# Optimization experiments

Measured on AMD Instinct MI355X. Metric: run time of the kernel, lower is better.

## Reference

```python
import jax, jax.numpy as jnp
import numpy as np

B, S, K, V = 512, 1024, 128, 512
SCALE = float(np.sqrt(K))


def setup_inputs() -> dict:
    key0 = jax.random.key(0)
    ks = jax.random.split(key0, 16)
    inp = {
        "keys": jax.random.normal(ks[0], (B, S, K), jnp.float32),
        "values": jax.random.normal(ks[1], (B, S, V), jnp.float32),
        "key": jax.random.normal(ks[2], (B, K), jnp.float32),
        "value": jax.random.normal(ks[3], (B, V), jnp.float32),
        "hidden": jax.random.normal(ks[4], (B, V), jnp.float32),
        "write_ptr": jax.random.randint(ks[5], (B,), 0, S, jnp.int64).astype(jnp.int64),
        "filled": jax.random.randint(ks[6], (B,), 0, S, jnp.int64).astype(jnp.int64),
        # parameters (Linear: y = x @ W.T + b)
        "Wq": jax.random.normal(ks[7], (K, V), jnp.float32) / np.sqrt(V),
        "bq": jnp.zeros((K,), jnp.float32),
        "Wg1": jax.random.normal(ks[8], (V, 2 * V), jnp.float32) / np.sqrt(2 * V),
        "bg1": jnp.zeros((V,), jnp.float32),
        "Wg2": jax.random.normal(ks[9], (V, V), jnp.float32) / np.sqrt(V),
        "bg2": jnp.zeros((V,), jnp.float32),
        "Wo": jax.random.normal(ks[10], (V, V), jnp.float32) / np.sqrt(V),
        "bo": jnp.zeros((V,), jnp.float32),
    }
    return inp


def reference(keys, values, key, value, hidden, write_ptr, filled,
              Wq, bq, Wg1, bg1, Wg2, bg2, Wo, bo):
    b_idx = jnp.arange(B)
    # --- write (ring-buffer scatter; torch does it under no_grad) ---
    keys_w = keys.at[b_idx, write_ptr].set(jax.lax.stop_gradient(key))
    values_w = values.at[b_idx, write_ptr].set(jax.lax.stop_gradient(value))
    filled_w = jnp.minimum(filled + 1, S)
    # --- read ---
    query = hidden @ Wq.T + bq                                  # (B, K)
    scores = jnp.einsum('bsk,bk->bs', keys_w, query) / SCALE     # (B, S)
    valid = jnp.arange(S)[None, :] < filled_w[:, None]           # (B, S)
    scores = jnp.where(valid, scores, -jnp.inf)
    attn = jax.nn.softmax(scores, axis=-1)
    attn = jnp.nan_to_num(attn, nan=0.0)
    retrieved = jnp.einsum('bs,bsv->bv', attn, values_w)         # (B, V)
    h_cat = jnp.concatenate([hidden, retrieved], axis=-1)        # (B, 2V)
    g = jax.nn.silu(h_cat @ Wg1.T + bg1)
    gate = jax.nn.sigmoid(g @ Wg2.T + bg2)
    out = (hidden + gate * retrieved) @ Wo.T + bo                # (B, V)
    return out
```

## Files before the change

kernel.cpp:

```cpp
#include <hip/hip_runtime.h>
#include <math.h>

#define BB 512
#define SS 1024
#define KK 128
#define VV 512
#define NC 4
#define CH 256

static constexpr float INV_SCALE = 0.088388347648318447f;

__global__ __launch_bounds__(128) void q_kernel(
    const float* __restrict__ hidden, const float* __restrict__ Wq,
    const float* __restrict__ bq, float* __restrict__ qout)
{
    __shared__ __align__(16) float hid[VV];
    const int b = blockIdx.x, t = threadIdx.x;
    ((float4*)hid)[t] = ((const float4*)(hidden + (size_t)b * VV))[t];
    __syncthreads();
    const float4* w4 = (const float4*)(Wq + (size_t)t * VV);
    const float4* h4 = (const float4*)hid;
    float acc = 0.f;
    #pragma unroll 8
    for (int v = 0; v < VV / 4; ++v) {
        float4 a = w4[v], h = h4[v];
        acc += a.x * h.x + a.y * h.y + a.z * h.z + a.w * h.w;
    }
    qout[(size_t)b * KK + t] = acc + bq[t];
}

__global__ __launch_bounds__(256) void transpose3_kernel(
    const float* __restrict__ Wg1, const float* __restrict__ Wg2,
    const float* __restrict__ Wo,
    float* __restrict__ wt1, float* __restrict__ wt2, float* __restrict__ wto)
{
    __shared__ float tile[32][33];
    const int idx = blockIdx.x;
    const float* in; float* out; int C, R, tid;
    if (idx < 512)      { in = Wg1; out = wt1; R = 512; C = 1024; tid = idx; }
    else if (idx < 768) { in = Wg2; out = wt2; R = 512; C = 512;  tid = idx - 512; }
    else                { in = Wo;  out = wto; R = 512; C = 512;  tid = idx - 768; }
    const int tiles_x = C >> 5;
    const int bx = (tid % tiles_x) << 5;
    const int by = (tid / tiles_x) << 5;
    const int tx = threadIdx.x & 31, ty0 = threadIdx.x >> 5;
    #pragma unroll
    for (int i = 0; i < 32; i += 8)
        tile[ty0 + i][tx] = in[(size_t)(by + ty0 + i) * C + bx + tx];
    __syncthreads();
    #pragma unroll
    for (int i = 0; i < 32; i += 8)
        out[(size_t)(bx + ty0 + i) * R + by + tx] = tile[tx][ty0 + i];
}

__global__ __launch_bounds__(256) void attn_chunk_kernel(
    const float* __restrict__ keys, const float* __restrict__ values,
    const float* __restrict__ keyv, const float* __restrict__ valv,
    const float* __restrict__ q,
    const int* __restrict__ write_ptr, const int* __restrict__ filled,
    float* __restrict__ ml, float* __restrict__ accp)
{
    __shared__ __align__(16) float qs[KK];
    __shared__ __align__(16) float p[CH];
    __shared__ __align__(16) float red[4];
    __shared__ __align__(16) float4 pvp[VV / 4];

    const int bc = blockIdx.x;
    const int b = bc >> 2;
    const int c = bc & 3;
    const int t = threadIdx.x;
    const int wave = t >> 6, lane = t & 63;

    int f = filled[b] + 1; if (f > SS) f = SS;
    const int sbeg = c * CH;
    int n = f - sbeg; if (n > CH) n = CH;

    float* mlrow = ml + ((size_t)b * NC + c) * 2;
    float* arow  = accp + ((size_t)b * NC + c) * VV;

    if (n <= 0) {
        if (t == 0) { mlrow[0] = -INFINITY; mlrow[1] = 0.f; }
        if (t < VV / 4) ((float4*)arow)[t] = make_float4(0.f, 0.f, 0.f, 0.f);
        return;
    }

    if (t < KK / 4) ((float4*)qs)[t] = ((const float4*)(q + (size_t)b * KK))[t];
    __syncthreads();

    const int sub = lane & 31, rsel = lane >> 5;
    const int srow = wave * 2 + rsel;
    const float4 q4 = ((const float4*)qs)[sub];
    const float* kb = keys + ((size_t)b * SS + sbeg) * KK;
    const float* kw = keyv + (size_t)b * KK;
    const int wpl = write_ptr[b] - sbeg;

    const int nmain = n & ~31;
    for (int s0 = 0; s0 < nmain; s0 += 32) {
        float4 kv[4];
        #pragma unroll
        for (int u = 0; u < 4; ++u) {
            const int s = s0 + u * 8 + srow;
            const float* kr = (s == wpl) ? kw : (kb + (size_t)s * KK);
            kv[u] = ((const float4*)kr)[sub];
        }
        #pragma unroll
        for (int u = 0; u < 4; ++u) {
            float prt = kv[u].x * q4.x + kv[u].y * q4.y
                      + kv[u].z * q4.z + kv[u].w * q4.w;
            prt += __shfl_xor(prt, 16);
            prt += __shfl_xor(prt, 8);
            prt += __shfl_xor(prt, 4);
            prt += __shfl_xor(prt, 2);
            prt += __shfl_xor(prt, 1);
            if (sub == 0) p[s0 + u * 8 + srow] = prt * INV_SCALE;
        }
    }
    for (int s = nmain + srow; s < n; s += 8) {
        const float* kr = (s == wpl) ? kw : (kb + (size_t)s * KK);
        const float4 kv = ((const float4*)kr)[sub];
        float prt = kv.x * q4.x + kv.y * q4.y + kv.z * q4.z + kv.w * q4.w;
        prt += __shfl_xor(prt, 16);
        prt += __shfl_xor(prt, 8);
        prt += __shfl_xor(prt, 4);
        prt += __shfl_xor(prt, 2);
        prt += __shfl_xor(prt, 1);
        if (sub == 0) p[s] = prt * INV_SCALE;
    }
    __syncthreads();

    float lmax = -INFINITY;
    for (int i = t; i < n; i += 256) lmax = fmaxf(lmax, p[i]);
    lmax = fmaxf(lmax, __shfl_xor(lmax, 32));
    lmax = fmaxf(lmax, __shfl_xor(lmax, 16));
    lmax = fmaxf(lmax, __shfl_xor(lmax, 8));
    lmax = fmaxf(lmax, __shfl_xor(lmax, 4));
    lmax = fmaxf(lmax, __shfl_xor(lmax, 2));
    lmax = fmaxf(lmax, __shfl_xor(lmax, 1));
    if (lane == 0) red[wave] = lmax;
    __syncthreads();
    const float m = fmaxf(fmaxf(red[0], red[1]), fmaxf(red[2], red[3]));
    float lsum = 0.f;
    for (int i = t; i < n; i += 256) {
        const float e = __expf(p[i] - m);
        p[i] = e;
        lsum += e;
    }
    lsum += __shfl_xor(lsum, 32);
    lsum += __shfl_xor(lsum, 16);
    lsum += __shfl_xor(lsum, 8);
    lsum += __shfl_xor(lsum, 4);
    lsum += __shfl_xor(lsum, 2);
    lsum += __shfl_xor(lsum, 1);
    __syncthreads();
    if (lane == 0) red[wave] = lsum;
    __syncthreads();
    const float l = red[0] + red[1] + red[2] + red[3];

    const int col4 = t & 127, stream = t >> 7;
    const float4* vb = (const float4*)(values + ((size_t)b * SS + sbeg) * VV);
    const float4* vw = (const float4*)(valv + (size_t)b * VV);
    float4 acc = make_float4(0.f, 0.f, 0.f, 0.f);
    const int nm2 = n & ~15;
    for (int s0 = 0; s0 < nm2; s0 += 16) {
        float4 v[8]; float ps[8];
        #pragma unroll
        for (int u = 0; u < 8; ++u) {
            const int s = s0 + u * 2 + stream;
            const float4* vr = (s == wpl) ? vw : (vb + (size_t)s * (VV / 4));
            v[u] = vr[col4];
            ps[u] = p[s];
        }
        #pragma unroll
        for (int u = 0; u < 8; ++u) {
            acc.x += ps[u] * v[u].x;
            acc.y += ps[u] * v[u].y;
            acc.z += ps[u] * v[u].z;
            acc.w += ps[u] * v[u].w;
        }
    }
    for (int s = nm2 + stream; s < n; s += 2) {
        const float4* vr = (s == wpl) ? vw : (vb + (size_t)s * (VV / 4));
        const float4 v = vr[col4];
        const float psv = p[s];
        acc.x += psv * v.x;
        acc.y += psv * v.y;
        acc.z += psv * v.z;
        acc.w += psv * v.w;
    }
    if (stream == 1) pvp[col4] = acc;
    __syncthreads();
    if (stream == 0) {
        const float4 o = pvp[col4];
        ((float4*)arow)[col4] = make_float4(acc.x + o.x, acc.y + o.y,
                                            acc.z + o.z, acc.w + o.w);
    }
    if (t == 0) { mlrow[0] = m; mlrow[1] = l; }
}

__global__ __launch_bounds__(128) void combine_kernel(
    const float* __restrict__ hidden, const float* __restrict__ ml,
    const float* __restrict__ accp, float* __restrict__ hcat)
{
    const int b = blockIdx.x, t = threadIdx.x;
    const float* mlb = ml + (size_t)b * NC * 2;
    const float m0 = mlb[0], l0 = mlb[1], m1 = mlb[2], l1 = mlb[3];
    const float m2 = mlb[4], l2 = mlb[5], m3 = mlb[6], l3 = mlb[7];
    const float ms = fmaxf(fmaxf(m0, m1), fmaxf(m2, m3));
    const float w0 = __expf(m0 - ms), w1 = __expf(m1 - ms);
    const float w2 = __expf(m2 - ms), w3 = __expf(m3 - ms);
    const float invd = 1.f / (w0 * l0 + w1 * l1 + w2 * l2 + w3 * l3);
    const float4 x0 = ((const float4*)(accp + ((size_t)b * NC + 0) * VV))[t];
    const float4 x1 = ((const float4*)(accp + ((size_t)b * NC + 1) * VV))[t];
    const float4 x2 = ((const float4*)(accp + ((size_t)b * NC + 2) * VV))[t];
    const float4 x3 = ((const float4*)(accp + ((size_t)b * NC + 3) * VV))[t];
    float4 r;
    r.x = (w0 * x0.x + w1 * x1.x + w2 * x2.x + w3 * x3.x) * invd;
    r.y = (w0 * x0.y + w1 * x1.y + w2 * x2.y + w3 * x3.y) * invd;
    r.z = (w0 * x0.z + w1 * x1.z + w2 * x2.z + w3 * x3.z) * invd;
    r.w = (w0 * x0.w + w1 * x1.w + w2 * x2.w + w3 * x3.w) * invd;
    float4* hc = (float4*)(hcat + (size_t)b * 2 * VV);
    hc[t] = ((const float4*)(hidden + (size_t)b * VV))[t];
    hc[VV / 4 + t] = r;
}

__global__ __launch_bounds__(256) void gemm_ks_kernel(
    const float* __restrict__ A, int K, const float* __restrict__ B,
    float* __restrict__ part)
{
    __shared__ __align__(16) float As[16][68];
    __shared__ __align__(16) float Bs[16][68];
    const int bx = blockIdx.x;
    const int mt = bx & 7, nt = (bx >> 3) & 7, ks = bx >> 6;
    const int kseg = K >> 2;
    const int kbeg = ks * kseg, kend = kbeg + kseg;
    const int t = threadIdx.x;
    const int tx = t & 15, ty = t >> 4;
    const int m0 = mt << 6, n0 = nt << 6;
    const int ra = t >> 2, ca = (t & 3) << 2;
    const int rb = t >> 4, jb = (t & 15) << 2;
    float4 a0 = {0,0,0,0}, a1 = {0,0,0,0}, a2 = {0,0,0,0}, a3 = {0,0,0,0};

    for (int k0 = kbeg; k0 < kend; k0 += 16) {
        const float4 av = *(const float4*)(A + (size_t)(m0 + ra) * K + k0 + ca);
        const float4 bv = *(const float4*)(B + (size_t)(k0 + rb) * VV + n0 + jb);
        As[ca + 0][ra] = av.x;
        As[ca + 1][ra] = av.y;
        As[ca + 2][ra] = av.z;
        As[ca + 3][ra] = av.w;
        *(float4*)&Bs[rb][jb] = bv;
        __syncthreads();
        #pragma unroll
        for (int k = 0; k < 16; ++k) {
            const float4 a = *(const float4*)&As[k][ty << 2];
            const float4 b = *(const float4*)&Bs[k][tx << 2];
            a0.x += a.x * b.x; a0.y += a.x * b.y; a0.z += a.x * b.z; a0.w += a.x * b.w;
            a1.x += a.y * b.x; a1.y += a.y * b.y; a1.z += a.y * b.z; a1.w += a.y * b.w;
            a2.x += a.z * b.x; a2.y += a.z * b.y; a2.z += a.z * b.z; a2.w += a.z * b.w;
            a3.x += a.w * b.x; a3.y += a.w * b.y; a3.z += a.w * b.z; a3.w += a.w * b.w;
        }
        __syncthreads();
    }
    float* pp = part + ((size_t)(ks * 512 + m0 + (ty << 2))) * 512 + n0 + (tx << 2);
    *(float4*)(pp + 0 * 512) = a0;
    *(float4*)(pp + 1 * 512) = a1;
    *(float4*)(pp + 2 * 512) = a2;
    *(float4*)(pp + 3 * 512) = a3;
}

__global__ __launch_bounds__(128) void reduce_silu_kernel(
    const float* __restrict__ part, const float* __restrict__ bg1,
    float* __restrict__ G)
{
    const int b = blockIdx.x, t = threadIdx.x;
    const size_t o = (size_t)b * (VV / 4) + t;
    const size_t st = (size_t)512 * (VV / 4);
    const float4* p4 = (const float4*)part;
    const float4 s0 = p4[o], s1 = p4[o + st], s2 = p4[o + 2 * st], s3 = p4[o + 3 * st];
    const float4 bb = ((const float4*)bg1)[t];
    float4 s;
    s.x = s0.x + s1.x + s2.x + s3.x + bb.x;
    s.y = s0.y + s1.y + s2.y + s3.y + bb.y;
    s.z = s0.z + s1.z + s2.z + s3.z + bb.z;
    s.w = s0.w + s1.w + s2.w + s3.w + bb.w;
    float4 g;
    g.x = s.x / (1.f + __expf(-s.x));
    g.y = s.y / (1.f + __expf(-s.y));
    g.z = s.z / (1.f + __expf(-s.z));
    g.w = s.w / (1.f + __expf(-s.w));
    ((float4*)G)[o] = g;
}

__global__ __launch_bounds__(128) void reduce_gate_kernel(
    const float* __restrict__ part, const float* __restrict__ bg2,
    const float* __restrict__ hcat, float* __restrict__ X)
{
    const int b = blockIdx.x, t = threadIdx.x;
    const size_t o = (size_t)b * (VV / 4) + t;
    const size_t st = (size_t)512 * (VV / 4);
    const float4* p4 = (const float4*)part;
    const float4 s0 = p4[o], s1 = p4[o + st], s2 = p4[o + 2 * st], s3 = p4[o + 3 * st];
    const float4 bb = ((const float4*)bg2)[t];
    float4 s;
    s.x = s0.x + s1.x + s2.x + s3.x + bb.x;
    s.y = s0.y + s1.y + s2.y + s3.y + bb.y;
    s.z = s0.z + s1.z + s2.z + s3.z + bb.z;
    s.w = s0.w + s1.w + s2.w + s3.w + bb.w;
    const float4* hc = (const float4*)(hcat + (size_t)b * 2 * VV);
    const float4 h = hc[t];
    const float4 r = hc[VV / 4 + t];
    float4 x;
    x.x = h.x + r.x / (1.f + __expf(-s.x));
    x.y = h.y + r.y / (1.f + __expf(-s.y));
    x.z = h.z + r.z / (1.f + __expf(-s.z));
    x.w = h.w + r.w / (1.f + __expf(-s.w));
    ((float4*)X)[o] = x;
}

__global__ __launch_bounds__(128) void reduce_bias_kernel(
    const float* __restrict__ part, const float* __restrict__ bo,
    float* __restrict__ out)
{
    const int b = blockIdx.x, t = threadIdx.x;
    const size_t o = (size_t)b * (VV / 4) + t;
    const size_t st = (size_t)512 * (VV / 4);
    const float4* p4 = (const float4*)part;
    const float4 s0 = p4[o], s1 = p4[o + st], s2 = p4[o + 2 * st], s3 = p4[o + 3 * st];
    const float4 bb = ((const float4*)bo)[t];
    float4 s;
    s.x = s0.x + s1.x + s2.x + s3.x + bb.x;
    s.y = s0.y + s1.y + s2.y + s3.y + bb.y;
    s.z = s0.z + s1.z + s2.z + s3.z + bb.z;
    s.w = s0.w + s1.w + s2.w + s3.w + bb.w;
    ((float4*)out)[o] = s;
}

extern "C" void kernel_launch(void* const* d_in, const int* in_sizes, int n_in,
                              void* d_out, int out_size, void* d_ws, size_t ws_size,
                              hipStream_t stream) {
    const float* keys    = (const float*)d_in[0];
    const float* values  = (const float*)d_in[1];
    const float* keyv    = (const float*)d_in[2];
    const float* valv    = (const float*)d_in[3];
    const float* hidden  = (const float*)d_in[4];
    const int*   wptr    = (const int*)d_in[5];
    const int*   filled  = (const int*)d_in[6];
    const float* Wq  = (const float*)d_in[7];
    const float* bq  = (const float*)d_in[8];
    const float* Wg1 = (const float*)d_in[9];
    const float* bg1 = (const float*)d_in[10];
    const float* Wg2 = (const float*)d_in[11];
    const float* bg2 = (const float*)d_in[12];
    const float* Wo  = (const float*)d_in[13];
    const float* bo  = (const float*)d_in[14];
    float* out = (float*)d_out;

    float* ws   = (float*)d_ws;
    float* q    = ws;
    float* ml   = q + (size_t)BB * KK;
    float* accp = ml + (size_t)BB * NC * 2;
    float* wt1  = accp + (size_t)BB * NC * VV;
    float* wt2  = wt1 + (size_t)2 * VV * VV;
    float* wto  = wt2 + (size_t)VV * VV;
    float* hcat = wto + (size_t)VV * VV;
    float* G    = hcat + (size_t)BB * 2 * VV;
    float* X    = G + (size_t)BB * VV;
    float* part = X + (size_t)BB * VV;

    q_kernel<<<BB, 128, 0, stream>>>(hidden, Wq, bq, q);
    transpose3_kernel<<<1024, 256, 0, stream>>>(Wg1, Wg2, Wo, wt1, wt2, wto);
    attn_chunk_kernel<<<BB * NC, 256, 0, stream>>>(keys, values, keyv, valv, q,
                                                   wptr, filled, ml, accp);
    combine_kernel<<<BB, 128, 0, stream>>>(hidden, ml, accp, hcat);

    gemm_ks_kernel<<<256, 256, 0, stream>>>(hcat, 2 * VV, wt1, part);
    reduce_silu_kernel<<<BB, 128, 0, stream>>>(part, bg1, G);

    gemm_ks_kernel<<<256, 256, 0, stream>>>(G, VV, wt2, part);
    reduce_gate_kernel<<<BB, 128, 0, stream>>>(part, bg2, hcat, X);

    gemm_ks_kernel<<<256, 256, 0, stream>>>(X, VV, wto, part);
    reduce_bias_kernel<<<BB, 128, 0, stream>>>(part, bo, out);
}
```

Measured before the change: 231.4 us.

## Fuse split-K reduction into GEMM via atomic counters, merge prep kernels, double chunks

Merges the Q projection and weight transposes into one prep kernel, with the Q dot product split across two halves per block. Attention chunks go from 4 to 8 per batch row, giving more blocks for the memory-bound scan. The GEMMs go from 4-way to 8-way split-K, and the last-arriving block per tile, detected with an atomic counter and threadfence, sums the partials and applies the bias, SiLU, gate or identity epilogue. This removes the three reduce kernel launches, at the cost of a larger partial buffer, an extra memset and serialized tail work in the last block of each tile.

```diff
diff --git a/kernel.cpp b/kernel.cpp
--- a/kernel.cpp
+++ b/kernel.cpp
@@ -5,52 +5,58 @@
 #define SS 1024
 #define KK 128
 #define VV 512
-#define NC 4
-#define CH 256
+#define NC 8
+#define CH 128
+#define KS 8
 
 static constexpr float INV_SCALE = 0.088388347648318447f;
 
-__global__ __launch_bounds__(128) void q_kernel(
+__global__ __launch_bounds__(256) void prep_kernel(
+    const float* __restrict__ Wg1, const float* __restrict__ Wg2,
+    const float* __restrict__ Wo,
+    float* __restrict__ wt1, float* __restrict__ wt2, float* __restrict__ wto,
     const float* __restrict__ hidden, const float* __restrict__ Wq,
     const float* __restrict__ bq, float* __restrict__ qout)
 {
+    __shared__ float tile[32][33];
     __shared__ __align__(16) float hid[VV];
-    const int b = blockIdx.x, t = threadIdx.x;
-    ((float4*)hid)[t] = ((const float4*)(hidden + (size_t)b * VV))[t];
-    __syncthreads();
-    const float4* w4 = (const float4*)(Wq + (size_t)t * VV);
-    const float4* h4 = (const float4*)hid;
-    float acc = 0.f;
-    #pragma unroll 8
-    for (int v = 0; v < VV / 4; ++v) {
-        float4 a = w4[v], h = h4[v];
-        acc += a.x * h.x + a.y * h.y + a.z * h.z + a.w * h.w;
-    }
-    qout[(size_t)b * KK + t] = acc + bq[t];
-}
-
-__global__ __launch_bounds__(256) void transpose3_kernel(
-    const float* __restrict__ Wg1, const float* __restrict__ Wg2,
-    const float* __restrict__ Wo,
-    float* __restrict__ wt1, float* __restrict__ wt2, float* __restrict__ wto)
-{
-    __shared__ float tile[32][33];
+    __shared__ float qp[2][KK];
     const int idx = blockIdx.x;
-    const float* in; float* out; int C, R, tid;
-    if (idx < 512)      { in = Wg1; out = wt1; R = 512; C = 1024; tid = idx; }
-    else if (idx < 768) { in = Wg2; out = wt2; R = 512; C = 512;  tid = idx - 512; }
-    else                { in = Wo;  out = wto; R = 512; C = 512;  tid = idx - 768; }
-    const int tiles_x = C >> 5;
-    const int bx = (tid % tiles_x) << 5;
-    const int by = (tid / tiles_x) << 5;
-    const int tx = threadIdx.x & 31, ty0 = threadIdx.x >> 5;
-    #pragma unroll
-    for (int i = 0; i < 32; i += 8)
-        tile[ty0 + i][tx] = in[(size_t)(by + ty0 + i) * C + bx + tx];
-    __syncthreads();
-    #pragma unroll
-    for (int i = 0; i < 32; i += 8)
-        out[(size_t)(bx + ty0 + i) * R + by + tx] = tile[tx][ty0 + i];
+    const int t = threadIdx.x;
+    if (idx < 1024) {
+        const float* in; float* out; int C, R, tid;
+        if (idx < 512)      { in = Wg1; out = wt1; R = 512; C = 1024; tid = idx; }
+        else if (idx < 768) { in = Wg2; out = wt2; R = 512; C = 512;  tid = idx - 512; }
+        else                { in = Wo;  out = wto; R = 512; C = 512;  tid = idx - 768; }
+        const int tiles_x = C >> 5;
+        const int bx = (tid % tiles_x) << 5;
+        const int by = (tid / tiles_x) << 5;
+        const int tx = t & 31, ty0 = t >> 5;
+        #pragma unroll
+        for (int i = 0; i < 32; i += 8)
+            tile[ty0 + i][tx] = in[(size_t)(by + ty0 + i) * C + bx + tx];
+        __syncthreads();
+        #pragma unroll
+        for (int i = 0; i < 32; i += 8)
+            out[(size_t)(bx + ty0 + i) * R + by + tx] = tile[tx][ty0 + i];
+    } else {
+        const int b = idx - 1024;
+        if (t < VV / 4)
+            ((float4*)hid)[t] = ((const float4*)(hidden + (size_t)b * VV))[t];
+        __syncthreads();
+        const int k = t & 127, half = t >> 7;
+        const float4* w4 = (const float4*)(Wq + (size_t)k * VV + half * 256);
+        const float4* h4 = (const float4*)(hid + half * 256);
+        float acc = 0.f;
+        #pragma unroll 8
+        for (int v = 0; v < 64; ++v) {
+            float4 a = w4[v], h = h4[v];
+            acc += a.x * h.x + a.y * h.y + a.z * h.z + a.w * h.w;
+        }
+        qp[half][k] = acc;
+        __syncthreads();
+        if (t < KK) qout[(size_t)b * KK + t] = qp[0][t] + qp[1][t] + bq[t];
+    }
 }
 
 __global__ __launch_bounds__(256) void attn_chunk_kernel(
@@ -66,8 +72,8 @@
     __shared__ __align__(16) float4 pvp[VV / 4];
 
     const int bc = blockIdx.x;
-    const int b = bc >> 2;
-    const int c = bc & 3;
+    const int b = bc >> 3;
+    const int c = bc & 7;
     const int t = threadIdx.x;
     const int wave = t >> 6, lane = t & 63;
 
@@ -203,35 +209,42 @@
 {
     const int b = blockIdx.x, t = threadIdx.x;
     const float* mlb = ml + (size_t)b * NC * 2;
-    const float m0 = mlb[0], l0 = mlb[1], m1 = mlb[2], l1 = mlb[3];
-    const float m2 = mlb[4], l2 = mlb[5], m3 = mlb[6], l3 = mlb[7];
-    const float ms = fmaxf(fmaxf(m0, m1), fmaxf(m2, m3));
-    const float w0 = __expf(m0 - ms), w1 = __expf(m1 - ms);
-    const float w2 = __expf(m2 - ms), w3 = __expf(m3 - ms);
-    const float invd = 1.f / (w0 * l0 + w1 * l1 + w2 * l2 + w3 * l3);
-    const float4 x0 = ((const float4*)(accp + ((size_t)b * NC + 0) * VV))[t];
-    const float4 x1 = ((const float4*)(accp + ((size_t)b * NC + 1) * VV))[t];
-    const float4 x2 = ((const float4*)(accp + ((size_t)b * NC + 2) * VV))[t];
-    const float4 x3 = ((const float4*)(accp + ((size_t)b * NC + 3) * VV))[t];
-    float4 r;
-    r.x = (w0 * x0.x + w1 * x1.x + w2 * x2.x + w3 * x3.x) * invd;
-    r.y = (w0 * x0.y + w1 * x1.y + w2 * x2.y + w3 * x3.y) * invd;
-    r.z = (w0 * x0.z + w1 * x1.z + w2 * x2.z + w3 * x3.z) * invd;
-    r.w = (w0 * x0.w + w1 * x1.w + w2 * x2.w + w3 * x3.w) * invd;
+    float mv[NC], lv[NC];
+    #pragma unroll
+    for (int c = 0; c < NC; ++c) { mv[c] = mlb[2 * c]; lv[c] = mlb[2 * c + 1]; }
+    float ms = mv[0];
+    #pragma unroll
+    for (int c = 1; c < NC; ++c) ms = fmaxf(ms, mv[c]);
+    float w[NC], denom = 0.f;
+    #pragma unroll
+    for (int c = 0; c < NC; ++c) { w[c] = __expf(mv[c] - ms); denom += w[c] * lv[c]; }
+    const float invd = 1.f / denom;
+    float4 r = make_float4(0.f, 0.f, 0.f, 0.f);
+    #pragma unroll
+    for (int c = 0; c < NC; ++c) {
+        const float4 x = ((const float4*)(accp + ((size_t)b * NC + c) * VV))[t];
+        r.x += w[c] * x.x; r.y += w[c] * x.y; r.z += w[c] * x.z; r.w += w[c] * x.w;
+    }
+    r.x *= invd; r.y *= invd; r.z *= invd; r.w *= invd;
     float4* hc = (float4*)(hcat + (size_t)b * 2 * VV);
     hc[t] = ((const float4*)(hidden + (size_t)b * VV))[t];
     hc[VV / 4 + t] = r;
 }
 
-__global__ __launch_bounds__(256) void gemm_ks_kernel(
+__global__ __launch_bounds__(256) void gemm_ep_kernel(
     const float* __restrict__ A, int K, const float* __restrict__ B,
-    float* __restrict__ part)
+    float* __restrict__ part, int* __restrict__ cnt,
+    const float* __restrict__ bias, const float* __restrict__ hcat,
+    float* __restrict__ dst, int epi)
 {
     __shared__ __align__(16) float As[16][68];
     __shared__ __align__(16) float Bs[16][68];
+    __shared__ int lastFlag;
     const int bx = blockIdx.x;
-    const int mt = bx & 7, nt = (bx >> 3) & 7, ks = bx >> 6;
-    const int kseg = K >> 2;
+    const int tile_id = bx & 63;
+    const int ks = bx >> 6;
+    const int mt = tile_id & 7, nt = tile_id >> 3;
+    const int kseg = K >> 3;
     const int kbeg = ks * kseg, kend = kbeg + kseg;
     const int t = threadIdx.x;
     const int tx = t & 15, ty = t >> 4;
@@ -260,78 +273,51 @@
         }
         __syncthreads();
     }
-    float* pp = part + ((size_t)(ks * 512 + m0 + (ty << 2))) * 512 + n0 + (tx << 2);
-    *(float4*)(pp + 0 * 512) = a0;
-    *(float4*)(pp + 1 * 512) = a1;
-    *(float4*)(pp + 2 * 512) = a2;
-    *(float4*)(pp + 3 * 512) = a3;
-}
-
-__global__ __launch_bounds__(128) void reduce_silu_kernel(
-    const float* __restrict__ part, const float* __restrict__ bg1,
-    float* __restrict__ G)
-{
-    const int b = blockIdx.x, t = threadIdx.x;
-    const size_t o = (size_t)b * (VV / 4) + t;
-    const size_t st = (size_t)512 * (VV / 4);
-    const float4* p4 = (const float4*)part;
-    const float4 s0 = p4[o], s1 = p4[o + st], s2 = p4[o + 2 * st], s3 = p4[o + 3 * st];
-    const float4 bb = ((const float4*)bg1)[t];
-    float4 s;
-    s.x = s0.x + s1.x + s2.x + s3.x + bb.x;
-    s.y = s0.y + s1.y + s2.y + s3.y + bb.y;
-    s.z = s0.z + s1.z + s2.z + s3.z + bb.z;
-    s.w = s0.w + s1.w + s2.w + s3.w + bb.w;
-    float4 g;
-    g.x = s.x / (1.f + __expf(-s.x));
-    g.y = s.y / (1.f + __expf(-s.y));
-    g.z = s.z / (1.f + __expf(-s.z));
-    g.w = s.w / (1.f + __expf(-s.w));
-    ((float4*)G)[o] = g;
-}
-
-__global__ __launch_bounds__(128) void reduce_gate_kernel(
-    const float* __restrict__ part, const float* __restrict__ bg2,
-    const float* __restrict__ hcat, float* __restrict__ X)
-{
-    const int b = blockIdx.x, t = threadIdx.x;
-    const size_t o = (size_t)b * (VV / 4) + t;
-    const size_t st = (size_t)512 * (VV / 4);
-    const float4* p4 = (const float4*)part;
-    const float4 s0 = p4[o], s1 = p4[o + st], s2 = p4[o + 2 * st], s3 = p4[o + 3 * st];
-    const float4 bb = ((const float4*)bg2)[t];
-    float4 s;
-    s.x = s0.x + s1.x + s2.x + s3.x + bb.x;
-    s.y = s0.y + s1.y + s2.y + s3.y + bb.y;
-    s.z = s0.z + s1.z + s2.z + s3.z + bb.z;
-    s.w = s0.w + s1.w + s2.w + s3.w + bb.w;
-    const float4* hc = (const float4*)(hcat + (size_t)b * 2 * VV);
-    const float4 h = hc[t];
-    const float4 r = hc[VV / 4 + t];
-    float4 x;
-    x.x = h.x + r.x / (1.f + __expf(-s.x));
-    x.y = h.y + r.y / (1.f + __expf(-s.y));
-    x.z = h.z + r.z / (1.f + __expf(-s.z));
-    x.w = h.w + r.w / (1.f + __expf(-s.w));
-    ((float4*)X)[o] = x;
-}
-
-__global__ __launch_bounds__(128) void reduce_bias_kernel(
-    const float* __restrict__ part, const float* __restrict__ bo,
-    float* __restrict__ out)
-{
-    const int b = blockIdx.x, t = threadIdx.x;
-    const size_t o = (size_t)b * (VV / 4) + t;
-    const size_t st = (size_t)512 * (VV / 4);
-    const float4* p4 = (const float4*)part;
-    const float4 s0 = p4[o], s1 = p4[o + st], s2 = p4[o + 2 * st], s3 = p4[o + 3 * st];
-    const float4 bb = ((const float4*)bo)[t];
-    float4 s;
-    s.x = s0.x + s1.x + s2.x + s3.x + bb.x;
-    s.y = s0.y + s1.y + s2.y + s3.y + bb.y;
-    s.z = s0.z + s1.z + s2.z + s3.z + bb.z;
-    s.w = s0.w + s1.w + s2.w + s3.w + bb.w;
-    ((float4*)out)[o] = s;
+    const size_t st = (size_t)VV * VV;
+    {
+        float* pp = part + (size_t)ks * st
+                  + (size_t)(m0 + (ty << 2)) * VV + n0 + (tx << 2);
+        *(float4*)(pp + 0 * VV) = a0;
+        *(float4*)(pp + 1 * VV) = a1;
+        *(float4*)(pp + 2 * VV) = a2;
+        *(float4*)(pp + 3 * VV) = a3;
+    }
+    __threadfence();
+    if (t == 0) lastFlag = (atomicAdd(&cnt[tile_id], 1) == KS - 1);
+    __syncthreads();
+    if (!lastFlag) return;
+    __threadfence();
+
+    const int col = n0 + (tx << 2);
+    const float4 bb = *(const float4*)(bias + col);
+    #pragma unroll
+    for (int r = 0; r < 4; ++r) {
+        const int row = m0 + (ty << 2) + r;
+        float4 s = bb;
+        #pragma unroll
+        for (int k2 = 0; k2 < KS; ++k2) {
+            const float4 pv = *(const float4*)(part + (size_t)k2 * st
+                                               + (size_t)row * VV + col);
+            s.x += pv.x; s.y += pv.y; s.z += pv.z; s.w += pv.w;
+        }
+        float4 o;
+        if (epi == 0) {
+            o.x = s.x / (1.f + __expf(-s.x));
+            o.y = s.y / (1.f + __expf(-s.y));
+            o.z = s.z / (1.f + __expf(-s.z));
+            o.w = s.w / (1.f + __expf(-s.w));
+        } else if (epi == 1) {
+            const float4 h  = *(const float4*)(hcat + (size_t)row * (2 * VV) + col);
+            const float4 rr = *(const float4*)(hcat + (size_t)row * (2 * VV) + VV + col);
+            o.x = h.x + rr.x / (1.f + __expf(-s.x));
+            o.y = h.y + rr.y / (1.f + __expf(-s.y));
+            o.z = h.z + rr.z / (1.f + __expf(-s.z));
+            o.w = h.w + rr.w / (1.f + __expf(-s.w));
+        } else {
+            o = s;
+        }
+        *(float4*)(dst + (size_t)row * VV + col) = o;
+    }
 }
 
 extern "C" void kernel_launch(void* const* d_in, const int* in_sizes, int n_in,
@@ -365,19 +351,19 @@
     float* G    = hcat + (size_t)BB * 2 * VV;
     float* X    = G + (size_t)BB * VV;
     float* part = X + (size_t)BB * VV;
-
-    q_kernel<<<BB, 128, 0, stream>>>(hidden, Wq, bq, q);
-    transpose3_kernel<<<1024, 256, 0, stream>>>(Wg1, Wg2, Wo, wt1, wt2, wto);
+    int*   cnt  = (int*)(part + (size_t)KS * VV * VV);
+
+    hipMemsetAsync(cnt, 0, 3 * 64 * sizeof(int), stream);
+    prep_kernel<<<1536, 256, 0, stream>>>(Wg1, Wg2, Wo, wt1, wt2, wto,
+                                          hidden, Wq, bq, q);
     attn_chunk_kernel<<<BB * NC, 256, 0, stream>>>(keys, values, keyv, valv, q,
                                                    wptr, filled, ml, accp);
     combine_kernel<<<BB, 128, 0, stream>>>(hidden, ml, accp, hcat);
 
-    gemm_ks_kernel<<<256, 256, 0, stream>>>(hcat, 2 * VV, wt1, part);
-    reduce_silu_kernel<<<BB, 128, 0, stream>>>(part, bg1, G);
-
-    gemm_ks_kernel<<<256, 256, 0, stream>>>(G, VV, wt2, part);
-    reduce_gate_kernel<<<BB, 128, 0, stream>>>(part, bg2, hcat, X);
-
-    gemm_ks_kernel<<<256, 256, 0, stream>>>(X, VV, wto, part);
-    reduce_bias_kernel<<<BB, 128, 0, stream>>>(part, bo, out);
-}
+    gemm_ep_kernel<<<64 * KS, 256, 0, stream>>>(hcat, 2 * VV, wt1, part,
+                                                cnt, bg1, nullptr, G, 0);
+    gemm_ep_kernel<<<64 * KS, 256, 0, stream>>>(G, VV, wt2, part,
+                                                cnt + 64, bg2, hcat, X, 1);
+    gemm_ep_kernel<<<64 * KS, 256, 0, stream>>>(X, VV, wto, part,
+                                                cnt + 128, bo, nullptr, out, 2);
+}
```

Measured after the change: 387.3 us. 67.4% more time.

## Split attention into 16 chunks and read GEMM weights untransposed

Applied to the files above, without the earlier changes.

Attention is now split into 16 chunks of 64 keys per batch row instead of 4 chunks of 256, which gives more blocks and better load balance across the variable fill lengths. The combine step is generalised to merge 16 partial softmax results. The weight transpose kernel is removed, and the GEMM loads each W row directly and transposes it into shared memory the same way it does for A. This drops one launch and the transpose traffic, at the cost of strided W loads, more partial buffers and a heavier combine.

```diff
diff --git a/kernel.cpp b/kernel.cpp
--- a/kernel.cpp
+++ b/kernel.cpp
@@ -5,8 +5,9 @@
 #define SS 1024
 #define KK 128
 #define VV 512
-#define NC 4
-#define CH 256
+#define NC 16
+#define CH 64
+#define KS 4
 
 static constexpr float INV_SCALE = 0.088388347648318447f;
 
@@ -29,30 +30,6 @@
     qout[(size_t)b * KK + t] = acc + bq[t];
 }
 
-__global__ __launch_bounds__(256) void transpose3_kernel(
-    const float* __restrict__ Wg1, const float* __restrict__ Wg2,
-    const float* __restrict__ Wo,
-    float* __restrict__ wt1, float* __restrict__ wt2, float* __restrict__ wto)
-{
-    __shared__ float tile[32][33];
-    const int idx = blockIdx.x;
-    const float* in; float* out; int C, R, tid;
-    if (idx < 512)      { in = Wg1; out = wt1; R = 512; C = 1024; tid = idx; }
-    else if (idx < 768) { in = Wg2; out = wt2; R = 512; C = 512;  tid = idx - 512; }
-    else                { in = Wo;  out = wto; R = 512; C = 512;  tid = idx - 768; }
-    const int tiles_x = C >> 5;
-    const int bx = (tid % tiles_x) << 5;
-    const int by = (tid / tiles_x) << 5;
-    const int tx = threadIdx.x & 31, ty0 = threadIdx.x >> 5;
-    #pragma unroll
-    for (int i = 0; i < 32; i += 8)
-        tile[ty0 + i][tx] = in[(size_t)(by + ty0 + i) * C + bx + tx];
-    __syncthreads();
-    #pragma unroll
-    for (int i = 0; i < 32; i += 8)
-        out[(size_t)(bx + ty0 + i) * R + by + tx] = tile[tx][ty0 + i];
-}
-
 __global__ __launch_bounds__(256) void attn_chunk_kernel(
     const float* __restrict__ keys, const float* __restrict__ values,
     const float* __restrict__ keyv, const float* __restrict__ valv,
@@ -66,8 +43,8 @@
     __shared__ __align__(16) float4 pvp[VV / 4];
 
     const int bc = blockIdx.x;
-    const int b = bc >> 2;
-    const int c = bc & 3;
+    const int b = bc >> 4;
+    const int c = bc & 15;
     const int t = threadIdx.x;
     const int wave = t >> 6, lane = t & 63;
 
@@ -203,28 +180,30 @@
 {
     const int b = blockIdx.x, t = threadIdx.x;
     const float* mlb = ml + (size_t)b * NC * 2;
-    const float m0 = mlb[0], l0 = mlb[1], m1 = mlb[2], l1 = mlb[3];
-    const float m2 = mlb[4], l2 = mlb[5], m3 = mlb[6], l3 = mlb[7];
-    const float ms = fmaxf(fmaxf(m0, m1), fmaxf(m2, m3));
-    const float w0 = __expf(m0 - ms), w1 = __expf(m1 - ms);
-    const float w2 = __expf(m2 - ms), w3 = __expf(m3 - ms);
-    const float invd = 1.f / (w0 * l0 + w1 * l1 + w2 * l2 + w3 * l3);
-    const float4 x0 = ((const float4*)(accp + ((size_t)b * NC + 0) * VV))[t];
-    const float4 x1 = ((const float4*)(accp + ((size_t)b * NC + 1) * VV))[t];
-    const float4 x2 = ((const float4*)(accp + ((size_t)b * NC + 2) * VV))[t];
-    const float4 x3 = ((const float4*)(accp + ((size_t)b * NC + 3) * VV))[t];
-    float4 r;
-    r.x = (w0 * x0.x + w1 * x1.x + w2 * x2.x + w3 * x3.x) * invd;
-    r.y = (w0 * x0.y + w1 * x1.y + w2 * x2.y + w3 * x3.y) * invd;
-    r.z = (w0 * x0.z + w1 * x1.z + w2 * x2.z + w3 * x3.z) * invd;
-    r.w = (w0 * x0.w + w1 * x1.w + w2 * x2.w + w3 * x3.w) * invd;
+    float mv[NC], lv[NC];
+    #pragma unroll
+    for (int c = 0; c < NC; ++c) { mv[c] = mlb[2 * c]; lv[c] = mlb[2 * c + 1]; }
+    float ms = mv[0];
+    #pragma unroll
+    for (int c = 1; c < NC; ++c) ms = fmaxf(ms, mv[c]);
+    float w[NC], denom = 0.f;
+    #pragma unroll
+    for (int c = 0; c < NC; ++c) { w[c] = __expf(mv[c] - ms); denom += w[c] * lv[c]; }
+    const float invd = 1.f / denom;
+    float4 r = make_float4(0.f, 0.f, 0.f, 0.f);
+    #pragma unroll
+    for (int c = 0; c < NC; ++c) {
+        const float4 x = ((const float4*)(accp + ((size_t)b * NC + c) * VV))[t];
+        r.x += w[c] * x.x; r.y += w[c] * x.y; r.z += w[c] * x.z; r.w += w[c] * x.w;
+    }
+    r.x *= invd; r.y *= invd; r.z *= invd; r.w *= invd;
     float4* hc = (float4*)(hcat + (size_t)b * 2 * VV);
     hc[t] = ((const float4*)(hidden + (size_t)b * VV))[t];
     hc[VV / 4 + t] = r;
 }
 
 __global__ __launch_bounds__(256) void gemm_ks_kernel(
-    const float* __restrict__ A, int K, const float* __restrict__ B,
+    const float* __restrict__ A, int K, const float* __restrict__ W,
     float* __restrict__ part)
 {
     __shared__ __align__(16) float As[16][68];
@@ -237,17 +216,19 @@
     const int tx = t & 15, ty = t >> 4;
     const int m0 = mt << 6, n0 = nt << 6;
     const int ra = t >> 2, ca = (t & 3) << 2;
-    const int rb = t >> 4, jb = (t & 15) << 2;
     float4 a0 = {0,0,0,0}, a1 = {0,0,0,0}, a2 = {0,0,0,0}, a3 = {0,0,0,0};
 
     for (int k0 = kbeg; k0 < kend; k0 += 16) {
         const float4 av = *(const float4*)(A + (size_t)(m0 + ra) * K + k0 + ca);
-        const float4 bv = *(const float4*)(B + (size_t)(k0 + rb) * VV + n0 + jb);
+        const float4 wv = *(const float4*)(W + (size_t)(n0 + ra) * K + k0 + ca);
         As[ca + 0][ra] = av.x;
         As[ca + 1][ra] = av.y;
         As[ca + 2][ra] = av.z;
         As[ca + 3][ra] = av.w;
-        *(float4*)&Bs[rb][jb] = bv;
+        Bs[ca + 0][ra] = wv.x;
+        Bs[ca + 1][ra] = wv.y;
+        Bs[ca + 2][ra] = wv.z;
+        Bs[ca + 3][ra] = wv.w;
         __syncthreads();
         #pragma unroll
         for (int k = 0; k < 16; ++k) {
@@ -358,26 +339,22 @@
     float* q    = ws;
     float* ml   = q + (size_t)BB * KK;
     float* accp = ml + (size_t)BB * NC * 2;
-    float* wt1  = accp + (size_t)BB * NC * VV;
-    float* wt2  = wt1 + (size_t)2 * VV * VV;
-    float* wto  = wt2 + (size_t)VV * VV;
-    float* hcat = wto + (size_t)VV * VV;
+    float* hcat = accp + (size_t)BB * NC * VV;
     float* G    = hcat + (size_t)BB * 2 * VV;
     float* X    = G + (size_t)BB * VV;
     float* part = X + (size_t)BB * VV;
 
     q_kernel<<<BB, 128, 0, stream>>>(hidden, Wq, bq, q);
-    transpose3_kernel<<<1024, 256, 0, stream>>>(Wg1, Wg2, Wo, wt1, wt2, wto);
     attn_chunk_kernel<<<BB * NC, 256, 0, stream>>>(keys, values, keyv, valv, q,
                                                    wptr, filled, ml, accp);
     combine_kernel<<<BB, 128, 0, stream>>>(hidden, ml, accp, hcat);
 
-    gemm_ks_kernel<<<256, 256, 0, stream>>>(hcat, 2 * VV, wt1, part);
+    gemm_ks_kernel<<<256, 256, 0, stream>>>(hcat, 2 * VV, Wg1, part);
     reduce_silu_kernel<<<BB, 128, 0, stream>>>(part, bg1, G);
 
-    gemm_ks_kernel<<<256, 256, 0, stream>>>(G, VV, wt2, part);
+    gemm_ks_kernel<<<256, 256, 0, stream>>>(G, VV, Wg2, part);
     reduce_gate_kernel<<<BB, 128, 0, stream>>>(part, bg2, hcat, X);
 
-    gemm_ks_kernel<<<256, 256, 0, stream>>>(X, VV, wto, part);
+    gemm_ks_kernel<<<256, 256, 0, stream>>>(X, VV, Wo, part);
     reduce_bias_kernel<<<BB, 128, 0, stream>>>(part, bo, out);
 }
```

Measured after the change: 223.8 us. -3.3%, faster.
